# Kernel tuning notes

Hardware: AMD Instinct MI355X
Metric: run time of the kernel (lower is better)

Reference implementation:

```python
import jax, jax.numpy as jnp
import numpy as np

SR = 44100.0
MIN_GAIN, MAX_GAIN = -48.0, 12.0
MIN_EQ, MAX_EQ = -15.0, 15.0
MIN_CTS, MAX_CTS = -20.0, 10.0
# Freeverb (JUCE Reverb, as used by pedalboard.Reverb) tunings @ 44.1 kHz
COMB_T = [1116, 1188, 1277, 1356, 1422, 1491, 1557, 1617]
AP_T = [556, 441, 341, 225]
COMB_OFF = [0]
for _L in COMB_T:
    COMB_OFF.append(COMB_OFF[-1] + _L)
AP_OFF = [0]
for _L in AP_T:
    AP_OFF.append(AP_OFF[-1] + _L)


def restore(x, lo, hi):
    # inverse of normalize-to-(0,1)
    return x * (hi - lo) + lo


def first_order(fc, kind):
    # bilinear-transform 1st-order HP/LP (pedalboard High/LowpassFilter are 1st order)
    K = jnp.tan(np.pi * fc / SR)
    a1 = (K - 1.0) / (K + 1.0)
    z = jnp.zeros_like(fc)
    if kind == "hp":
        b0 = 1.0 / (1.0 + K)
        b = jnp.stack([b0, -b0, z], -1)
    else:
        b0 = K / (1.0 + K)
        b = jnp.stack([b0, b0, z], -1)
    a = jnp.stack([jnp.ones_like(fc), a1, z], -1)
    return b, a


def shelf(fc, gain_db, high):
    # RBJ cookbook shelf, Q = 1/sqrt(2)
    A = 10.0 ** (gain_db / 40.0)
    w = 2.0 * np.pi * fc / SR
    cw = jnp.cos(w)
    alpha = jnp.sin(w) * (np.sqrt(2.0) / 2.0)
    sq = 2.0 * jnp.sqrt(A) * alpha
    s = 1.0 if high else -1.0
    b0 = A * ((A + 1.0) + s * (A - 1.0) * cw + sq)
    b1 = -2.0 * s * A * ((A - 1.0) + s * (A + 1.0) * cw)
    b2 = A * ((A + 1.0) + s * (A - 1.0) * cw - sq)
    a0 = (A + 1.0) - s * (A - 1.0) * cw + sq
    a1 = 2.0 * s * ((A - 1.0) - s * (A + 1.0) * cw)
    a2 = (A + 1.0) - s * (A - 1.0) * cw - sq
    return jnp.stack([b0, b1, b2], -1), jnp.stack([a0, a1, a2], -1)


def peak(fc, gain_db, q):
    # RBJ cookbook peaking EQ
    A = 10.0 ** (gain_db / 40.0)
    w = 2.0 * np.pi * fc / SR
    cw = jnp.cos(w)
    alpha = jnp.sin(w) / (2.0 * q)
    b = jnp.stack([1.0 + alpha * A, -2.0 * cw, 1.0 - alpha * A], -1)
    a = jnp.stack([1.0 + alpha / A, -2.0 * cw, 1.0 - alpha / A], -1)
    return b, a


def cascade_biquads(x, B, A):
    # x: [N, T]; B, A: [N, 6, 3]. DF2T cascade of 6 sections via one scan.
    B = B / A[..., :1]
    A = A / A[..., :1]
    n_sec = B.shape[1]

    def step(z, xt):  # z: [N, 6, 2], xt: [N]
        s = xt
        zn = []
        for k in range(n_sec):
            y = B[:, k, 0] * s + z[:, k, 0]
            z1 = B[:, k, 1] * s - A[:, k, 1] * y + z[:, k, 1]
            z2 = B[:, k, 2] * s - A[:, k, 2] * y
            zn.append(jnp.stack([z1, z2], -1))
            s = y
        return jnp.stack(zn, 1), s

    z0 = jnp.zeros((x.shape[0], n_sec, 2), x.dtype)
    _, y = jax.lax.scan(step, z0, x.T)
    return y.T


def compressor(x, thr_db, ratio, att_ms, rel_ms):
    # feed-forward compressor, dB-domain gain computer + one-pole attack/release
    a_att = jnp.exp(-1.0 / (att_ms * 1e-3 * SR))  # [N]
    a_rel = jnp.exp(-1.0 / (rel_ms * 1e-3 * SR))
    lvl = 20.0 * jnp.log10(jnp.abs(x) + 1e-6)  # [N, T]
    tgt = jnp.minimum(0.0, (thr_db[:, None] - lvl) * (1.0 - 1.0 / ratio[:, None]))

    def step(g, t):  # g, t: [N] gain reduction in dB (<= 0)
        coef = jnp.where(t < g, a_att, a_rel)
        g = coef * g + (1.0 - coef) * t
        return g, g

    _, g = jax.lax.scan(step, jnp.zeros(x.shape[0], x.dtype), tgt.T)
    return x * 10.0 ** (g.T / 20.0)


def freeverb(x, room, damp01, wet, dry, width):
    # JUCE/Freeverb mono: 8 parallel damped combs -> 4 series allpasses
    fb = room * 0.28 + 0.7
    damp = damp01 * 0.4
    wet1 = 3.0 * wet * 0.5 * (1.0 + width)
    dryg = 2.0 * dry
    N = x.shape[0]
    CL, AL = COMB_OFF[-1], AP_OFF[-1]

    def step(carry, xt):
        cb, ab, st, t = carry
        inp = xt * 0.015
        acc = jnp.zeros_like(xt)
        st_new = []
        for k in range(8):
            idx = COMB_OFF[k] + t % COMB_T[k]
            out = cb[:, idx]
            s = out * (1.0 - damp) + st[:, k] * damp
            cb = cb.at[:, idx].set(inp + s * fb)
            st_new.append(s)
            acc = acc + out
        for k in range(4):
            idx = AP_OFF[k] + t % AP_T[k]
            buf = ab[:, idx]
            ab = ab.at[:, idx].set(acc + buf * 0.5)
            acc = buf - acc
        y = acc * wet1 + xt * dryg
        return (cb, ab, jnp.stack(st_new, 1), t + 1), y

    carry0 = (jnp.zeros((N, CL), x.dtype), jnp.zeros((N, AL), x.dtype),
              jnp.zeros((N, 8), x.dtype), jnp.int32(0))
    _, y = jax.lax.scan(step, carry0, x.T)
    return y.T


def _forward(x, p):
    bs, nt, T = x.shape
    N = bs * nt
    xf = x.reshape(N, T)
    pf = p.reshape(N, 24)

    gain_in = restore(pf[:, 0], MIN_GAIN, MAX_GAIN)
    xf = xf * (10.0 ** (gain_in / 20.0))[:, None]

    hp_fc = restore(pf[:, 1], 0.0, 350.0)
    lp_fc = restore(pf[:, 2], 3000.0, 22000.0)
    hs_fc = restore(pf[:, 3], 1500.0, 16000.0)
    hs_g = restore(pf[:, 4], MIN_EQ, MAX_EQ)
    ls_fc = restore(pf[:, 5], 30.0, 450.0)
    ls_g = restore(pf[:, 6], MIN_EQ, MAX_EQ)
    mh_fc = restore(pf[:, 7], 600.0, 7000.0)
    mh_g = restore(pf[:, 8], MIN_EQ, MAX_EQ)
    mh_q = restore(pf[:, 9], 0.5, 3.0)
    ml_fc = restore(pf[:, 10], 200.0, 2500.0)
    ml_g = restore(pf[:, 11], MIN_EQ, MAX_EQ)
    ml_q = restore(pf[:, 12], 0.5, 3.0)
    c_thr = restore(pf[:, 13], MIN_CTS, MAX_CTS)
    c_rat = restore(pf[:, 14], 1.0, 20.0)
    c_att = restore(pf[:, 15], 1.0, 30.0)
    c_rel = restore(pf[:, 16], 100.0, 4000.0)

    coefs = [first_order(hp_fc, "hp"), first_order(lp_fc, "lp"),
             shelf(hs_fc, hs_g, True), shelf(ls_fc, ls_g, False),
             peak(mh_fc, mh_g, mh_q), peak(ml_fc, ml_g, ml_q)]
    B = jnp.stack([c[0] for c in coefs], 1)  # [N, 6, 3]
    A = jnp.stack([c[1] for c in coefs], 1)
    xf = cascade_biquads(xf, B, A)
    xf = compressor(xf, c_thr, c_rat, c_att, c_rel)
    xf = freeverb(xf, pf[:, 17], pf[:, 18], pf[:, 19], pf[:, 20], pf[:, 21])

    gain_out = restore(pf[:, 22], MIN_GAIN, MAX_GAIN)
    xf = xf * (10.0 ** (gain_out / 20.0))[:, None]

    pan = restore(pf[:, 23], 0.3, 0.7)
    theta = pan * (np.pi / 2.0)
    pang = jnp.stack([jnp.cos(theta), jnp.sin(theta)], -1).reshape(bs, nt, 2)
    y = jnp.einsum("bnt,bnc->bct", xf.reshape(bs, nt, T), pang)

    p_out = jnp.stack([gain_in, hp_fc, lp_fc, hs_fc, hs_g, ls_fc, ls_g,
                       mh_fc, mh_g, mh_q, ml_fc, ml_g, ml_q,
                       c_thr, c_rat, c_att, c_rel,
                       pf[:, 17], pf[:, 18], pf[:, 19], pf[:, 20], pf[:, 21],
                       gain_out, pan], -1).reshape(bs, nt, 24)
    return y, p_out


_forward_jit = jax.jit(_forward)


def setup_inputs() -> dict:
    key = jax.random.key(0)
    k1, k2 = jax.random.split(key)
    x = 0.1 * jax.random.normal(k1, (4, 8, 65536), dtype=jnp.float32)
    p = jax.random.uniform(k2, (4, 8, 24), dtype=jnp.float32)
    return {"x": x, "p": p}


def reference(x, p):
    return _forward_jit(x, p)
```

## Files before the change

kernel.cpp:

```cpp
#include <hip/hip_runtime.h>
#include <math.h>

#define T 65536
#define NCH 32
#define LCHUNK 512
#define CCHUNK 128
#define SB 256
#define NBLK 256
#define VH 8

#define OFS_A  0
#define OFS_B1 2097152
#define OFS_I  4194304
#define OFS_P  7340032
#define OFS_M  7342080
#define OFS_V  7346688
#define OFS_Z  7395840


__device__ void norm_store(double b0,double b1,double b2,double a0,double a1,double a2,
                           double* B, double* A1, double* A2, int k){
  B[k*3+0]=b0/a0; B[k*3+1]=b1/a0; B[k*3+2]=b2/a0; A1[k]=a1/a0; A2[k]=a2/a0;
}

__device__ void shelf_coefs(double fc, double g, double s, double* B, double* A1, double* A2, int k){
  double A  = pow(10.0, g/40.0);
  double w  = 2.0*3.14159265358979323846*fc/44100.0;
  double cw = cos(w);
  double al = sin(w)*0.70710678118654752;
  double sq = 2.0*sqrt(A)*al;
  double b0 = A*((A+1.0) + s*(A-1.0)*cw + sq);
  double b1 = -2.0*s*A*((A-1.0) + s*(A+1.0)*cw);
  double b2 = A*((A+1.0) + s*(A-1.0)*cw - sq);
  double a0 = (A+1.0) - s*(A-1.0)*cw + sq;
  double a1 = 2.0*s*((A-1.0) - s*(A+1.0)*cw);
  double a2 = (A+1.0) - s*(A-1.0)*cw - sq;
  norm_store(b0,b1,b2,a0,a1,a2,B,A1,A2,k);
}

__device__ void peak_coefs(double fc, double g, double q, double* B, double* A1, double* A2, int k){
  double A  = pow(10.0, g/40.0);
  double w  = 2.0*3.14159265358979323846*fc/44100.0;
  double cw = cos(w);
  double al = sin(w)/(2.0*q);
  norm_store(1.0+al*A, -2.0*cw, 1.0-al*A, 1.0+al/A, -2.0*cw, 1.0-al/A, B,A1,A2,k);
}

__global__ void k_params(const float* __restrict__ p, float* __restrict__ ws, float* __restrict__ pout){
  int ch = threadIdx.x;
  if (ch >= NCH) return;
  const float* pf = p + ch*24;
  float f[24];
  #pragma unroll
  for (int j=0;j<24;j++) f[j]=pf[j];

  double gain_in = (double)f[0]*60.0 - 48.0;
  double hp_fc  = (double)f[1]*350.0;
  double lp_fc  = (double)f[2]*19000.0 + 3000.0;
  double hs_fc  = (double)f[3]*14500.0 + 1500.0;
  double hs_g   = (double)f[4]*30.0 - 15.0;
  double ls_fc  = (double)f[5]*420.0 + 30.0;
  double ls_g   = (double)f[6]*30.0 - 15.0;
  double mh_fc  = (double)f[7]*6400.0 + 600.0;
  double mh_g   = (double)f[8]*30.0 - 15.0;
  double mh_q   = (double)f[9]*2.5 + 0.5;
  double ml_fc  = (double)f[10]*2300.0 + 200.0;
  double ml_g   = (double)f[11]*30.0 - 15.0;
  double ml_q   = (double)f[12]*2.5 + 0.5;
  double c_thr  = (double)f[13]*30.0 - 20.0;
  double c_rat  = (double)f[14]*19.0 + 1.0;
  double c_att  = (double)f[15]*29.0 + 1.0;
  double c_rel  = (double)f[16]*3900.0 + 100.0;
  double gain_out=(double)f[22]*60.0 - 48.0;
  double pan    = (double)f[23]*0.4 + 0.3;

  double B[18], A1[6], A2[6];
  { double K = tan(3.14159265358979323846*hp_fc/44100.0);
    double a1=(K-1.0)/(K+1.0), b0=1.0/(1.0+K);
    B[0]=b0; B[1]=-b0; B[2]=0.0; A1[0]=a1; A2[0]=0.0; }
  { double K = tan(3.14159265358979323846*lp_fc/44100.0);
    double a1=(K-1.0)/(K+1.0), b0=K/(1.0+K);
    B[3]=b0; B[4]=b0; B[5]=0.0; A1[1]=a1; A2[1]=0.0; }
  shelf_coefs(hs_fc, hs_g,  1.0, B, A1, A2, 2);
  shelf_coefs(ls_fc, ls_g, -1.0, B, A1, A2, 3);
  peak_coefs (mh_fc, mh_g, mh_q, B, A1, A2, 4);
  peak_coefs (ml_fc, ml_g, ml_q, B, A1, A2, 5);

  double gin = pow(10.0, gain_in/20.0);
  B[0]*=gin; B[1]*=gin; B[2]*=gin;

  float* Pc = ws + OFS_P + ch*64;
  #pragma unroll
  for (int k=0;k<6;k++){
    Pc[k]    = (float)B[k*3+0];
    Pc[6+k]  = (float)B[k*3+1];
    Pc[12+k] = (float)B[k*3+2];
    Pc[18+k] = (float)A1[k];
    Pc[24+k] = (float)A2[k];
  }
  Pc[30] = (float)c_thr;
  Pc[31] = (float)(1.0 - 1.0/c_rat);
  Pc[32] = (float)exp(-1.0/(c_att*0.001*44100.0));
  Pc[33] = (float)exp(-1.0/(c_rel*0.001*44100.0));
  double fb   = (double)f[17]*0.28 + 0.7;
  double damp = (double)f[18]*0.4;
  double wet1 = 3.0*(double)f[19]*0.5*(1.0+(double)f[21]);
  double dryg = 2.0*(double)f[20];
  double gout = pow(10.0, gain_out/20.0);
  Pc[34] = (float)fb;
  Pc[35] = (float)damp;
  Pc[36] = (float)(wet1*gout);
  Pc[37] = (float)(dryg*gout/0.015);
  Pc[38] = (float)cos(pan*1.57079632679489662);
  Pc[39] = (float)sin(pan*1.57079632679489662);

  float* po = pout + ch*24;
  po[0]=(float)gain_in; po[1]=(float)hp_fc; po[2]=(float)lp_fc; po[3]=(float)hs_fc;
  po[4]=(float)hs_g; po[5]=(float)ls_fc; po[6]=(float)ls_g; po[7]=(float)mh_fc;
  po[8]=(float)mh_g; po[9]=(float)mh_q; po[10]=(float)ml_fc; po[11]=(float)ml_g;
  po[12]=(float)ml_q; po[13]=(float)c_thr; po[14]=(float)c_rat; po[15]=(float)c_att;
  po[16]=(float)c_rel; po[17]=f[17]; po[18]=f[18]; po[19]=f[19]; po[20]=f[20];
  po[21]=f[21]; po[22]=(float)gain_out; po[23]=(float)pan;
}


__device__ __forceinline__ float bq_step(const float* b0, const float* b1, const float* b2,
                                         const float* a1, const float* a2,
                                         float* z1, float* z2, float s){
  #pragma unroll
  for (int k=0;k<6;k++){
    float y = fmaf(b0[k], s, z1[k]);
    z1[k] = fmaf(b1[k], s, fmaf(-a1[k], y, z2[k]));
    z2[k] = fmaf(b2[k], s, -a2[k]*y);
    s = y;
  }
  return s;
}

__device__ __forceinline__ void load_coefs(const float* Pc, float* b0, float* b1, float* b2,
                                           float* a1, float* a2){
  #pragma unroll
  for (int k=0;k<6;k++){
    b0[k]=Pc[k]; b1[k]=Pc[6+k]; b2[k]=Pc[12+k]; a1[k]=Pc[18+k]; a2[k]=Pc[24+k];
  }
}

__global__ void k_chunk1(const float* __restrict__ x, float* __restrict__ ws){
  int tg = blockIdx.x*64 + threadIdx.x;
  int ch = tg / 140, sub = tg % 140;
  if (ch >= NCH) return;
  const float* Pc = ws + OFS_P + ch*64;
  float b0[6],b1[6],b2[6],a1[6],a2[6];
  load_coefs(Pc,b0,b1,b2,a1,a2);
  float z1[6]={0,0,0,0,0,0}, z2[6]={0,0,0,0,0,0};

  if (sub < CCHUNK){
    const float4* xp = (const float4*)(x + ch*T + sub*LCHUNK);
    for (int j=0;j<LCHUNK/4;j++){
      float4 v = xp[j];
      bq_step(b0,b1,b2,a1,a2,z1,z2,v.x);
      bq_step(b0,b1,b2,a1,a2,z1,z2,v.y);
      bq_step(b0,b1,b2,a1,a2,z1,z2,v.z);
      bq_step(b0,b1,b2,a1,a2,z1,z2,v.w);
    }
    float* vo = ws + OFS_V + (ch*CCHUNK + sub)*12;
    #pragma unroll
    for (int k=0;k<6;k++){ vo[2*k]=z1[k]; vo[2*k+1]=z2[k]; }
  } else {
    int j = sub - CCHUNK;
    if ((j & 1)==0) z1[j>>1]=1.0f; else z2[j>>1]=1.0f;
    for (int t=0;t<LCHUNK;t++) bq_step(b0,b1,b2,a1,a2,z1,z2,0.0f);
    float* mo = ws + OFS_M + ch*144 + j*12;
    #pragma unroll
    for (int k=0;k<6;k++){ mo[2*k]=z1[k]; mo[2*k+1]=z2[k]; }
  }
}

__global__ void k_chunk2(float* __restrict__ ws){
  int ch = threadIdx.x;
  if (ch >= NCH) return;
  const float* M = ws + OFS_M + ch*144;
  const float* V = ws + OFS_V + ch*CCHUNK*12;
  float*       Z = ws + OFS_Z + ch*CCHUNK*12;
  float z[12];
  #pragma unroll
  for (int i=0;i<12;i++) z[i]=0.0f;
  for (int c=0;c<CCHUNK;c++){
    #pragma unroll
    for (int i=0;i<12;i++) Z[c*12+i]=z[i];
    float zn[12];
    #pragma unroll
    for (int i=0;i<12;i++) zn[i]=V[c*12+i];
    #pragma unroll
    for (int j=0;j<12;j++){
      float zj = z[j];
      #pragma unroll
      for (int i=0;i<12;i++) zn[i] = fmaf(M[j*12+i], zj, zn[i]);
    }
    #pragma unroll
    for (int i=0;i<12;i++) z[i]=zn[i];
  }
}

__global__ void k_chunk3(const float* __restrict__ x, float* __restrict__ ws){
  int tg = blockIdx.x*64 + threadIdx.x;
  int ch = tg >> 7, c = tg & (CCHUNK-1);
  const float* Pc = ws + OFS_P + ch*64;
  float b0[6],b1[6],b2[6],a1[6],a2[6];
  load_coefs(Pc,b0,b1,b2,a1,a2);
  float thr = Pc[30], rt = Pc[31];
  float aA = Pc[32], aR = Pc[33];
  float kA = 1.0f - aA, kR = 1.0f - aR;
  const float* Zi = ws + OFS_Z + (ch*CCHUNK + c)*12;
  float z1[6], z2[6];
  #pragma unroll
  for (int k=0;k<6;k++){ z1[k]=Zi[2*k]; z2[k]=Zi[2*k+1]; }
  const float4* xp = (const float4*)(x + ch*T + c*LCHUNK);
  float4* Ao  = (float4*)(ws + OFS_A  + (size_t)ch*T + c*LCHUNK);
  float4* B1o = (float4*)(ws + OFS_B1 + (size_t)ch*T + c*LCHUNK);
  float*  Ig  = ws + OFS_I + (size_t)ch*98304;

  for (int gg=0; gg<64; gg++){
    float4 v0 = xp[2*gg], v1 = xp[2*gg+1];
    float ya[8], Tv[8];
    ya[0]=bq_step(b0,b1,b2,a1,a2,z1,z2,v0.x);
    ya[1]=bq_step(b0,b1,b2,a1,a2,z1,z2,v0.y);
    ya[2]=bq_step(b0,b1,b2,a1,a2,z1,z2,v0.z);
    ya[3]=bq_step(b0,b1,b2,a1,a2,z1,z2,v0.w);
    ya[4]=bq_step(b0,b1,b2,a1,a2,z1,z2,v1.x);
    ya[5]=bq_step(b0,b1,b2,a1,a2,z1,z2,v1.y);
    ya[6]=bq_step(b0,b1,b2,a1,a2,z1,z2,v1.z);
    ya[7]=bq_step(b0,b1,b2,a1,a2,z1,z2,v1.w);
    #pragma unroll
    for (int s=0;s<8;s++)
      Tv[s] = fminf(0.0f, (thr - 6.0205999132796239f*log2f(fabsf(ya[s])+1e-6f))*rt);
    Ao[2*gg]   = make_float4(ya[0],ya[1],ya[2],ya[3]);
    Ao[2*gg+1] = make_float4(ya[4],ya[5],ya[6],ya[7]);
    B1o[2*gg]   = make_float4(Tv[0],Tv[1],Tv[2],Tv[3]);
    B1o[2*gg+1] = make_float4(Tv[4],Tv[5],Tv[6],Tv[7]);
    float bb[9];
    bb[0] = kR*Tv[0]; bb[1] = kA*Tv[0];
    #pragma unroll
    for (int s=1;s<8;s++){
      float bA = kA*Tv[s], bR = kR*Tv[s];
      bb[s+1] = fmaf(aA, bb[s], bA);
      #pragma unroll
      for (int j=7;j>=1;j--){
        if (j<=s) bb[j] = fminf(fmaf(aA, bb[j-1], bA), fmaf(aR, bb[j], bR));
      }
      bb[0] = fmaf(aR, bb[0], bR);
    }
    int G = c*64 + gg;
    float* ig = Ig + (G>>5)*384 + (G&31)*12;
    *(float4*)(ig)   = make_float4(bb[0],bb[1],bb[2],bb[3]);
    *(float4*)(ig+4) = make_float4(bb[4],bb[5],bb[6],bb[7]);
    *(float4*)(ig+8) = make_float4(bb[8],0.0f,0.0f,0.0f);
  }
}


__global__ __launch_bounds__(320) void k_verb(float* __restrict__ ws){
  const int LC[8] = {1116,1188,1277,1356,1422,1491,1557,1617};
  const int COFF[8] = {0,1116,2304,3581,4937,6359,7850,9407};
  const int LA[4] = {556,441,341,225};
  const int AOFF[4] = {0,556,997,1338};
  int ch = blockIdx.x, tid = threadIdx.x;
  __shared__ float cb[11024];
  __shared__ float ab[1563];
  __shared__ float cH[8][264];
  __shared__ float xts[256];
  __shared__ float B1st[2][256];
  __shared__ float IldS[384];
  __shared__ float gB[2][32];
  __shared__ float xfer[32];
  const float* Pc = ws + OFS_P + ch*64;
  float fb = Pc[34], damp = Pc[35], wet1 = Pc[36], dryk = Pc[37];
  float aA = Pc[32], aR = Pc[33];
  float kA = 1.0f - aA, kR = 1.0f - aR;
  float omd = 1.0f - damp;
  float* Aio = ws + OFS_A + (size_t)ch*T;
  const float* B1c = ws + OFS_B1 + (size_t)ch*T;
  const float* IG  = ws + OFS_I + (size_t)ch*98304;
  for (int i=tid;i<11024;i+=320) cb[i]=0.0f;
  for (int i=tid;i<1563;i+=320)  ab[i]=0.0f;
  for (int i=tid;i<8*264;i+=320) ((float*)cH)[i]=0.0f;
  bool scanw = (tid >= 256);
  int sl = tid - 256;
  float w[VH];
  { float pw = 1.0f;
    #pragma unroll
    for (int d=0;d<VH;d++){ w[d]=pw; pw*=damp; } }
  float sj[9];
  { float pA = 1.0f;
    #pragma unroll
    for (int j=0;j<9;j++){ sj[j]=pA; pA*=aA; }
    float pR = 1.0f;
    #pragma unroll
    for (int j=8;j>=0;j--){ sj[j]*=pR; pR*=aR; } }
  int cbb[8] = {0,0,0,0,0,0,0,0};
  int abb[4] = {0,0,0,0};
  float gcarry = 0.0f;
  float4 iR0, iR1, bR;
  float xv = 0.0f;

  if (scanw){
    const float4* isrc = (const float4*)(IG);
    float4* idst = (float4*)IldS;
    idst[sl] = isrc[sl];
    if (sl < 32) idst[64+sl] = isrc[64+sl];
    iR0 = isrc[96+sl];
    if (sl < 32) iR1 = isrc[96+64+sl];
    const float4* bsrc = (const float4*)(B1c);
    ((float4*)B1st[0])[sl] = bsrc[sl];
    ((float4*)B1st[1])[sl] = bsrc[64+sl];
  }
  if (tid < 256) xv = Aio[tid];
  __syncthreads();
  if (tid == 256){
    float g = 0.0f;
    for (int m=0;m<32;m++){
      gB[0][m] = g;
      const float* Ip = &IldS[m*12];
      float f0=fmaf(sj[0],g,Ip[0]), f1=fmaf(sj[1],g,Ip[1]), f2=fmaf(sj[2],g,Ip[2]);
      float f3=fmaf(sj[3],g,Ip[3]), f4=fmaf(sj[4],g,Ip[4]), f5=fmaf(sj[5],g,Ip[5]);
      float f6=fmaf(sj[6],g,Ip[6]), f7=fmaf(sj[7],g,Ip[7]), f8=fmaf(sj[8],g,Ip[8]);
      g = fminf(fminf(fminf(f0,f1),fminf(f2,f3)),
                fminf(fminf(f4,f5),fminf(fminf(f6,f7),f8)));
    }
    gcarry = g;
  }
  __syncthreads();

  for (int i=0;i<NBLK;i++){
    int t0 = i<<8;
    int p = i & 1;
    float xt = 0.0f, acc = 0.0f, a = 0.0f;
    if (tid < 256){
      int m = tid>>3, r = tid&7;
      float g = gB[p][m];
      const float* Bl = B1st[p] + (m<<3);
      float4 q0 = *(const float4*)(Bl);
      float4 q1 = *(const float4*)(Bl+4);
      float tv[8] = {q0.x,q0.y,q0.z,q0.w,q1.x,q1.y,q1.z,q1.w};
      #pragma unroll
      for (int s=0;s<8;s++){
        if (s<=r){
          float tt = tv[s];
          g = fminf(fmaf(aA,g,kA*tt), fmaf(aR,g,kR*tt));
        }
      }
      xt = xv * exp2f(g*0.16609640474436813f) * 0.015f;
      xts[tid] = xt;
      #pragma unroll
      for (int k=0;k<8;k++){
        int idx = cbb[k]+tid; if (idx>=LC[k]) idx-=LC[k];
        float o = cb[COFF[k]+idx];
        cH[k][VH+tid] = omd*o;
        acc += o;
      }
    } else if (i+1 < NBLK){
      float4* idst = (float4*)IldS;
      idst[sl] = iR0;
      if (sl < 32) idst[64+sl] = iR1;
      if (i >= 1) ((float4*)B1st[(i+1)&1])[sl] = bR;
    }
    __syncthreads();
    if (tid < 256){
      if (i+1 < NBLK) xv = Aio[t0+256+tid];
      #pragma unroll
      for (int k=0;k<8;k++){
        float s = 0.0f;
        #pragma unroll
        for (int d=0;d<VH;d++) s = fmaf(w[d], cH[k][VH+tid-d], s);
        int idx = cbb[k]+tid; if (idx>=LC[k]) idx-=LC[k];
        cb[COFF[k]+idx] = fmaf(fb, s, xt);
      }
      a = acc;
      #pragma unroll
      for (int j=0;j<3;j++){
        int idx = abb[j]+tid; if (idx>=LA[j]) idx-=LA[j];
        float bv = ab[AOFF[j]+idx];
        ab[AOFF[j]+idx] = fmaf(0.5f, bv, a);
        a = bv - a;
      }
      if (tid >= 225) xfer[tid-225] = a;
    } else {
      if (i+2 < NBLK){
        const float4* isrc = (const float4*)(IG + (size_t)(i+2)*384);
        iR0 = isrc[sl];
        if (sl < 32) iR1 = isrc[64+sl];
        const float4* bsrc = (const float4*)(B1c + (size_t)(i+2)*SB);
        bR = bsrc[sl];
      }
      if (tid == 256 && i+1 < NBLK){
        int q = (i+1)&1;
        float g = gcarry;
        #pragma unroll 4
        for (int m=0;m<32;m++){
          gB[q][m] = g;
          const float* Ip = &IldS[m*12];
          float f0=fmaf(sj[0],g,Ip[0]), f1=fmaf(sj[1],g,Ip[1]), f2=fmaf(sj[2],g,Ip[2]);
          float f3=fmaf(sj[3],g,Ip[3]), f4=fmaf(sj[4],g,Ip[4]), f5=fmaf(sj[5],g,Ip[5]);
          float f6=fmaf(sj[6],g,Ip[6]), f7=fmaf(sj[7],g,Ip[7]), f8=fmaf(sj[8],g,Ip[8]);
          g = fminf(fminf(fminf(f0,f1),fminf(f2,f3)),
                    fminf(fminf(f4,f5),fminf(fminf(f6,f7),f8)));
        }
        gcarry = g;
      }
    }
    __syncthreads();
    if (tid < 225){
      int idx = abb[3]+tid; if (idx>=225) idx-=225;
      float bv = ab[AOFF[3]+idx];
      float b  = fmaf(0.5f, bv, a);
      float y  = bv - a;
      Aio[t0+tid] = fmaf(y, wet1, xts[tid]*dryk);
      if (tid < 31){
        float a2 = xfer[tid];
        float y2 = b - a2;
        ab[AOFF[3]+idx] = fmaf(0.5f, b, a2);
        Aio[t0+225+tid] = fmaf(y2, wet1, xts[225+tid]*dryk);
      } else {
        ab[AOFF[3]+idx] = b;
      }
    } else if (tid >= 232 && tid < 288){
      int q = tid-232; int k = q/7, d = q%7;
      cH[k][1+d] = cH[k][257+d];
    }
    #pragma unroll
    for (int k=0;k<8;k++){ cbb[k]+=SB; if (cbb[k]>=LC[k]) cbb[k]-=LC[k]; }
    #pragma unroll
    for (int j=0;j<4;j++){
      abb[j]+=SB;
      if (abb[j]>=LA[j]) abb[j]-=LA[j];
      if (abb[j]>=LA[j]) abb[j]-=LA[j];
    }
    __syncthreads();
  }
}


__global__ void k_mix(const float* __restrict__ ws, float* __restrict__ out){
  int id = blockIdx.x*256 + threadIdx.x;
  int t = id & (T-1), b = id >> 16;
  const float* Av = ws + OFS_A + (size_t)b*8*T + t;
  const float* P = ws + OFS_P;
  float s0=0.0f, s1=0.0f;
  #pragma unroll
  for (int n=0;n<8;n++){
    float v = Av[(size_t)n*T];
    int ch = b*8+n;
    s0 = fmaf(v, P[ch*64+38], s0);
    s1 = fmaf(v, P[ch*64+39], s1);
  }
  out[b*2*T + t]     = s0;
  out[b*2*T + T + t] = s1;
}

extern "C" void kernel_launch(void* const* d_in, const int* in_sizes, int n_in,
                              void* d_out, int out_size, void* d_ws, size_t ws_size,
                              hipStream_t stream) {
  const float* x = (const float*)d_in[0];
  const float* p = (const float*)d_in[1];
  float* out = (float*)d_out;
  float* ws  = (float*)d_ws;

  k_params<<<1, 64, 0, stream>>>(p, ws, out + 4*2*T);
  k_chunk1<<<70, 64, 0, stream>>>(x, ws);
  k_chunk2<<<1, 64, 0, stream>>>(ws);
  k_chunk3<<<64, 64, 0, stream>>>(x, ws);
  k_verb  <<<NCH, 320, 0, stream>>>(ws);
  k_mix   <<<(4*T)/256, 256, 0, stream>>>(ws, out);
}
```

Before: 962.5 us.

## Restructure reverb block loop to two barriers with padded comb buffers and split scan

Result: slower. 1.087 ms (+13.0%).

```diff
diff --git a/kernel.cpp b/kernel.cpp
--- a/kernel.cpp
+++ b/kernel.cpp
@@ -145,7 +145,7 @@
   }
 }
 
-__global__ void k_chunk1(const float* __restrict__ x, float* __restrict__ ws){
+__global__ __launch_bounds__(64,1) void k_chunk1(const float* __restrict__ x, float* __restrict__ ws){
   int tg = blockIdx.x*64 + threadIdx.x;
   int ch = tg / 140, sub = tg % 140;
   if (ch >= NCH) return;
@@ -176,33 +176,42 @@
   }
 }
 
-__global__ void k_chunk2(float* __restrict__ ws){
+__global__ __launch_bounds__(64,1) void k_chunk2(float* __restrict__ ws){
   int ch = threadIdx.x;
   if (ch >= NCH) return;
   const float* M = ws + OFS_M + ch*144;
   const float* V = ws + OFS_V + ch*CCHUNK*12;
   float*       Z = ws + OFS_Z + ch*CCHUNK*12;
-  float z[12];
+  float Mr[144];
+  #pragma unroll
+  for (int i=0;i<144;i++) Mr[i]=M[i];
+  float z[12], vbuf[12];
   #pragma unroll
   for (int i=0;i<12;i++) z[i]=0.0f;
+  #pragma unroll
+  for (int i=0;i<12;i++) vbuf[i]=V[i];
   for (int c=0;c<CCHUNK;c++){
     #pragma unroll
     for (int i=0;i<12;i++) Z[c*12+i]=z[i];
     float zn[12];
     #pragma unroll
-    for (int i=0;i<12;i++) zn[i]=V[c*12+i];
+    for (int i=0;i<12;i++) zn[i]=vbuf[i];
+    if (c+1<CCHUNK){
+      #pragma unroll
+      for (int i=0;i<12;i++) vbuf[i]=V[(c+1)*12+i];
+    }
     #pragma unroll
     for (int j=0;j<12;j++){
       float zj = z[j];
       #pragma unroll
-      for (int i=0;i<12;i++) zn[i] = fmaf(M[j*12+i], zj, zn[i]);
+      for (int i=0;i<12;i++) zn[i] = fmaf(Mr[j*12+i], zj, zn[i]);
     }
     #pragma unroll
     for (int i=0;i<12;i++) z[i]=zn[i];
   }
 }
 
-__global__ void k_chunk3(const float* __restrict__ x, float* __restrict__ ws){
+__global__ __launch_bounds__(64,1) void k_chunk3(const float* __restrict__ x, float* __restrict__ ws){
   int tg = blockIdx.x*64 + threadIdx.x;
   int ch = tg >> 7, c = tg & (CCHUNK-1);
   const float* Pc = ws + OFS_P + ch*64;
@@ -259,20 +268,33 @@
 }
 
 
+__device__ __forceinline__ float scan_run(const float* I, const float* sj, float g,
+                                          float* grow, int m0, int m1){
+  #pragma unroll 4
+  for (int m=m0;m<m1;m++){
+    grow[m]=g;
+    const float* Ip=&I[m*12];
+    float f0=fmaf(sj[0],g,Ip[0]), f1=fmaf(sj[1],g,Ip[1]), f2=fmaf(sj[2],g,Ip[2]);
+    float f3=fmaf(sj[3],g,Ip[3]), f4=fmaf(sj[4],g,Ip[4]), f5=fmaf(sj[5],g,Ip[5]);
+    float f6=fmaf(sj[6],g,Ip[6]), f7=fmaf(sj[7],g,Ip[7]), f8=fmaf(sj[8],g,Ip[8]);
+    g = fminf(fminf(fminf(f0,f1),fminf(f2,f3)),
+              fminf(fminf(f4,f5),fminf(fminf(f6,f7),f8)));
+  }
+  return g;
+}
+
 __global__ __launch_bounds__(320) void k_verb(float* __restrict__ ws){
   const int LC[8] = {1116,1188,1277,1356,1422,1491,1557,1617};
-  const int COFF[8] = {0,1116,2304,3581,4937,6359,7850,9407};
+  const int CPF[8] = {0,1124,2320,3605,4969,6399,7898,9463};
   const int LA[4] = {556,441,341,225};
   const int AOFF[4] = {0,556,997,1338};
   int ch = blockIdx.x, tid = threadIdx.x;
-  __shared__ float cb[11024];
+  __shared__ float cb[11088];
   __shared__ float ab[1563];
-  __shared__ float cH[8][264];
-  __shared__ float xts[256];
+  __shared__ float haloS[2][8][8];
   __shared__ float B1st[2][256];
   __shared__ float IldS[384];
-  __shared__ float gB[2][32];
-  __shared__ float xfer[32];
+  __shared__ float gB[3][32];
   const float* Pc = ws + OFS_P + ch*64;
   float fb = Pc[34], damp = Pc[35], wet1 = Pc[36], dryk = Pc[37];
   float aA = Pc[32], aR = Pc[33];
@@ -281,13 +303,13 @@
   float* Aio = ws + OFS_A + (size_t)ch*T;
   const float* B1c = ws + OFS_B1 + (size_t)ch*T;
   const float* IG  = ws + OFS_I + (size_t)ch*98304;
-  for (int i=tid;i<11024;i+=320) cb[i]=0.0f;
+  for (int i=tid;i<11088;i+=320) cb[i]=0.0f;
   for (int i=tid;i<1563;i+=320)  ab[i]=0.0f;
-  for (int i=tid;i<8*264;i+=320) ((float*)cH)[i]=0.0f;
+  if (tid < 128) ((float*)haloS)[tid]=0.0f;
   bool scanw = (tid >= 256);
   int sl = tid - 256;
   float w[VH];
-  { float pw = 1.0f;
+  { float pw = omd;
     #pragma unroll
     for (int d=0;d<VH;d++){ w[d]=pw; pw*=damp; } }
   float sj[9];
@@ -301,43 +323,47 @@
   int abb[4] = {0,0,0,0};
   float gcarry = 0.0f;
   float4 iR0, iR1, bR;
-  float xv = 0.0f;
+  float xv = 0.0f, xvn = 0.0f;
+  float aH = 0.0f, xtH = 0.0f; int idxH = 0;
 
   if (scanw){
     const float4* isrc = (const float4*)(IG);
     float4* idst = (float4*)IldS;
     idst[sl] = isrc[sl];
     if (sl < 32) idst[64+sl] = isrc[64+sl];
-    iR0 = isrc[96+sl];
-    if (sl < 32) iR1 = isrc[96+64+sl];
     const float4* bsrc = (const float4*)(B1c);
     ((float4*)B1st[0])[sl] = bsrc[sl];
     ((float4*)B1st[1])[sl] = bsrc[64+sl];
-  }
-  if (tid < 256) xv = Aio[tid];
+    if (sl == 0) gcarry = scan_run(IldS, sj, 0.0f, gB[0], 0, 32);
+    idst[sl] = isrc[96+sl];
+    if (sl < 32) idst[64+sl] = isrc[96+64+sl];
+    if (sl == 0) gcarry = scan_run(IldS, sj, gcarry, gB[1], 0, 32);
+    iR0 = isrc[192+sl];
+    if (sl < 32) iR1 = isrc[192+64+sl];
+    bR = ((const float4*)(B1c + 2*SB))[sl];
+  } else {
+    xv = Aio[tid];
+  }
   __syncthreads();
-  if (tid == 256){
-    float g = 0.0f;
-    for (int m=0;m<32;m++){
-      gB[0][m] = g;
-      const float* Ip = &IldS[m*12];
-      float f0=fmaf(sj[0],g,Ip[0]), f1=fmaf(sj[1],g,Ip[1]), f2=fmaf(sj[2],g,Ip[2]);
-      float f3=fmaf(sj[3],g,Ip[3]), f4=fmaf(sj[4],g,Ip[4]), f5=fmaf(sj[5],g,Ip[5]);
-      float f6=fmaf(sj[6],g,Ip[6]), f7=fmaf(sj[7],g,Ip[7]), f8=fmaf(sj[8],g,Ip[8]);
-      g = fminf(fminf(fminf(f0,f1),fminf(f2,f3)),
-                fminf(fminf(f4,f5),fminf(fminf(f6,f7),f8)));
-    }
-    gcarry = g;
-  }
-  __syncthreads();
-
+
+  int pr = 0, pw2 = 2;
   for (int i=0;i<NBLK;i++){
     int t0 = i<<8;
     int p = i & 1;
-    float xt = 0.0f, acc = 0.0f, a = 0.0f;
+    float acc = 0.0f, xt = 0.0f, a = 0.0f, outv = 0.0f, nb4v = 0.0f;
+    float wv[8]; int qk[8];
+    float nb1=0.f, nb2=0.f, nb3=0.f, bv4=0.f;
+    int idx1=0, idx2=0, idx3=0, idx4=0;
     if (tid < 256){
+      if (i > 0 && tid >= 225){
+        float bv = ab[AOFF[3]+idxH];
+        float y  = bv - aH;
+        ab[AOFF[3]+idxH] = fmaf(0.5f, bv, aH);
+        Aio[t0-256+tid] = fmaf(y, wet1, xtH*dryk);
+      }
+      if (i+1 < NBLK) xvn = Aio[t0+256+tid];
       int m = tid>>3, r = tid&7;
-      float g = gB[p][m];
+      float g = gB[pr][m];
       const float* Bl = B1st[p] + (m<<3);
       float4 q0 = *(const float4*)(Bl);
       float4 q1 = *(const float4*)(Bl+4);
@@ -350,82 +376,86 @@
         }
       }
       xt = xv * exp2f(g*0.16609640474436813f) * 0.015f;
-      xts[tid] = xt;
       #pragma unroll
       for (int k=0;k<8;k++){
-        int idx = cbb[k]+tid; if (idx>=LC[k]) idx-=LC[k];
-        float o = cb[COFF[k]+idx];
-        cH[k][VH+tid] = omd*o;
+        int slot = cbb[k]+tid; if (slot>=LC[k]) slot-=LC[k];
+        int q = CPF[k] + 8 + slot;
+        qk[k] = q;
+        const float* bp = &cb[q-7];
+        float f0=bp[0],f1=bp[1],f2=bp[2],f3=bp[3],f4=bp[4],f5=bp[5],f6=bp[6],f7=bp[7];
+        if (tid < 7){
+          f0 = haloS[p][k][tid];
+          if (tid<6) f1 = haloS[p][k][tid+1];
+          if (tid<5) f2 = haloS[p][k][tid+2];
+          if (tid<4) f3 = haloS[p][k][tid+3];
+          if (tid<3) f4 = haloS[p][k][tid+4];
+          if (tid<2) f5 = haloS[p][k][tid+5];
+          if (tid<1) f6 = haloS[p][k][tid+6];
+        }
+        float o = f7;
         acc += o;
-      }
-    } else if (i+1 < NBLK){
-      float4* idst = (float4*)IldS;
-      idst[sl] = iR0;
-      if (sl < 32) idst[64+sl] = iR1;
-      if (i >= 1) ((float4*)B1st[(i+1)&1])[sl] = bR;
+        float s = (fmaf(w[0],f7,w[1]*f6) + fmaf(w[2],f5,w[3]*f4))
+                + (fmaf(w[4],f3,w[5]*f2) + fmaf(w[6],f1,w[7]*f0));
+        wv[k] = fmaf(fb, s, xt);
+        if (tid >= 249) haloS[p^1][k][tid-249] = o;
+      }
+      idx1 = abb[0]+tid; if (idx1>=LA[0]) idx1-=LA[0];
+      idx2 = abb[1]+tid; if (idx2>=LA[1]) idx2-=LA[1];
+      idx3 = abb[2]+tid; if (idx3>=LA[2]) idx3-=LA[2];
+      idx4 = abb[3]+tid; if (idx4>=225) idx4-=225; if (idx4>=225) idx4-=225;
+      float bv1 = ab[AOFF[0]+idx1];
+      float bv2 = ab[AOFF[1]+idx2];
+      float bv3 = ab[AOFF[2]+idx3];
+      if (tid < 194) bv4 = ab[AOFF[3]+idx4];
+      a = acc;
+      nb1 = fmaf(0.5f, bv1, a); a = bv1 - a;
+      nb2 = fmaf(0.5f, bv2, a); a = bv2 - a;
+      nb3 = fmaf(0.5f, bv3, a); a = bv3 - a;
+      if (tid < 194){
+        nb4v = fmaf(0.5f, bv4, a);
+        float y = bv4 - a;
+        outv = fmaf(y, wet1, xt*dryk);
+      }
+    } else {
+      if (i+2 < NBLK){
+        float4* idst = (float4*)IldS;
+        idst[sl] = iR0;
+        if (sl < 32) idst[64+sl] = iR1;
+      }
+      if (i >= 1 && i+1 < NBLK) ((float4*)B1st[(i+1)&1])[sl] = bR;
+      if (tid == 256 && i+2 < NBLK) gcarry = scan_run(IldS, sj, gcarry, gB[pw2], 0, 16);
     }
     __syncthreads();
     if (tid < 256){
-      if (i+1 < NBLK) xv = Aio[t0+256+tid];
       #pragma unroll
       for (int k=0;k<8;k++){
-        float s = 0.0f;
-        #pragma unroll
-        for (int d=0;d<VH;d++) s = fmaf(w[d], cH[k][VH+tid-d], s);
-        int idx = cbb[k]+tid; if (idx>=LC[k]) idx-=LC[k];
-        cb[COFF[k]+idx] = fmaf(fb, s, xt);
-      }
-      a = acc;
-      #pragma unroll
-      for (int j=0;j<3;j++){
-        int idx = abb[j]+tid; if (idx>=LA[j]) idx-=LA[j];
-        float bv = ab[AOFF[j]+idx];
-        ab[AOFF[j]+idx] = fmaf(0.5f, bv, a);
-        a = bv - a;
-      }
-      if (tid >= 225) xfer[tid-225] = a;
+        cb[qk[k]] = wv[k];
+        int slot = qk[k] - CPF[k] - 8;
+        if (slot >= LC[k]-7) cb[qk[k]-LC[k]] = wv[k];
+      }
+      ab[AOFF[0]+idx1] = nb1;
+      ab[AOFF[1]+idx2] = nb2;
+      ab[AOFF[2]+idx3] = nb3;
+      if (tid < 194){
+        ab[AOFF[3]+idx4] = nb4v;
+        Aio[t0+tid] = outv;
+      } else if (tid < 225){
+        float bv = ab[AOFF[3]+idx4];
+        float y  = bv - a;
+        ab[AOFF[3]+idx4] = fmaf(0.5f, bv, a);
+        Aio[t0+tid] = fmaf(y, wet1, xt*dryk);
+      } else {
+        aH = a; idxH = idx4; xtH = xt;
+      }
+      xv = xvn;
     } else {
-      if (i+2 < NBLK){
-        const float4* isrc = (const float4*)(IG + (size_t)(i+2)*384);
+      if (i+3 < NBLK){
+        const float4* isrc = (const float4*)(IG + (size_t)(i+3)*384);
         iR0 = isrc[sl];
         if (sl < 32) iR1 = isrc[64+sl];
-        const float4* bsrc = (const float4*)(B1c + (size_t)(i+2)*SB);
-        bR = bsrc[sl];
-      }
-      if (tid == 256 && i+1 < NBLK){
-        int q = (i+1)&1;
-        float g = gcarry;
-        #pragma unroll 4
-        for (int m=0;m<32;m++){
-          gB[q][m] = g;
-          const float* Ip = &IldS[m*12];
-          float f0=fmaf(sj[0],g,Ip[0]), f1=fmaf(sj[1],g,Ip[1]), f2=fmaf(sj[2],g,Ip[2]);
-          float f3=fmaf(sj[3],g,Ip[3]), f4=fmaf(sj[4],g,Ip[4]), f5=fmaf(sj[5],g,Ip[5]);
-          float f6=fmaf(sj[6],g,Ip[6]), f7=fmaf(sj[7],g,Ip[7]), f8=fmaf(sj[8],g,Ip[8]);
-          g = fminf(fminf(fminf(f0,f1),fminf(f2,f3)),
-                    fminf(fminf(f4,f5),fminf(fminf(f6,f7),f8)));
-        }
-        gcarry = g;
-      }
-    }
-    __syncthreads();
-    if (tid < 225){
-      int idx = abb[3]+tid; if (idx>=225) idx-=225;
-      float bv = ab[AOFF[3]+idx];
-      float b  = fmaf(0.5f, bv, a);
-      float y  = bv - a;
-      Aio[t0+tid] = fmaf(y, wet1, xts[tid]*dryk);
-      if (tid < 31){
-        float a2 = xfer[tid];
-        float y2 = b - a2;
-        ab[AOFF[3]+idx] = fmaf(0.5f, b, a2);
-        Aio[t0+225+tid] = fmaf(y2, wet1, xts[225+tid]*dryk);
-      } else {
-        ab[AOFF[3]+idx] = b;
-      }
-    } else if (tid >= 232 && tid < 288){
-      int q = tid-232; int k = q/7, d = q%7;
-      cH[k][1+d] = cH[k][257+d];
+      }
+      if (i+2 < NBLK) bR = ((const float4*)(B1c + (size_t)(i+2)*SB))[sl];
+      if (tid == 256 && i+2 < NBLK) gcarry = scan_run(IldS, sj, gcarry, gB[pw2], 16, 32);
     }
     #pragma unroll
     for (int k=0;k<8;k++){ cbb[k]+=SB; if (cbb[k]>=LC[k]) cbb[k]-=LC[k]; }
@@ -435,7 +465,14 @@
       if (abb[j]>=LA[j]) abb[j]-=LA[j];
       if (abb[j]>=LA[j]) abb[j]-=LA[j];
     }
+    pr++; if (pr==3) pr=0;
+    pw2++; if (pw2==3) pw2=0;
     __syncthreads();
+  }
+  if (tid >= 225 && tid < 256){
+    float bv = ab[AOFF[3]+idxH];
+    float y  = bv - aH;
+    Aio[((NBLK-1)<<8)+tid] = fmaf(y, wet1, xtH*dryk);
   }
 }
 
```

## Pack two reverb channels per block and cache transition matrix in registers

Applied to the files above, without the earlier changes.

New measurement: 1.317 ms. 36.8% more time.

```diff
diff --git a/kernel.cpp b/kernel.cpp
--- a/kernel.cpp
+++ b/kernel.cpp
@@ -145,7 +145,7 @@
   }
 }
 
-__global__ void k_chunk1(const float* __restrict__ x, float* __restrict__ ws){
+__global__ __launch_bounds__(64,1) void k_chunk1(const float* __restrict__ x, float* __restrict__ ws){
   int tg = blockIdx.x*64 + threadIdx.x;
   int ch = tg / 140, sub = tg % 140;
   if (ch >= NCH) return;
@@ -176,33 +176,42 @@
   }
 }
 
-__global__ void k_chunk2(float* __restrict__ ws){
+__global__ __launch_bounds__(64,1) void k_chunk2(float* __restrict__ ws){
   int ch = threadIdx.x;
   if (ch >= NCH) return;
   const float* M = ws + OFS_M + ch*144;
   const float* V = ws + OFS_V + ch*CCHUNK*12;
   float*       Z = ws + OFS_Z + ch*CCHUNK*12;
-  float z[12];
+  float Mr[144];
+  #pragma unroll
+  for (int i=0;i<144;i++) Mr[i]=M[i];
+  float z[12], vbuf[12];
   #pragma unroll
   for (int i=0;i<12;i++) z[i]=0.0f;
+  #pragma unroll
+  for (int i=0;i<12;i++) vbuf[i]=V[i];
   for (int c=0;c<CCHUNK;c++){
     #pragma unroll
     for (int i=0;i<12;i++) Z[c*12+i]=z[i];
     float zn[12];
     #pragma unroll
-    for (int i=0;i<12;i++) zn[i]=V[c*12+i];
+    for (int i=0;i<12;i++) zn[i]=vbuf[i];
+    if (c+1<CCHUNK){
+      #pragma unroll
+      for (int i=0;i<12;i++) vbuf[i]=V[(c+1)*12+i];
+    }
     #pragma unroll
     for (int j=0;j<12;j++){
       float zj = z[j];
       #pragma unroll
-      for (int i=0;i<12;i++) zn[i] = fmaf(M[j*12+i], zj, zn[i]);
+      for (int i=0;i<12;i++) zn[i] = fmaf(Mr[j*12+i], zj, zn[i]);
     }
     #pragma unroll
     for (int i=0;i<12;i++) z[i]=zn[i];
   }
 }
 
-__global__ void k_chunk3(const float* __restrict__ x, float* __restrict__ ws){
+__global__ __launch_bounds__(64,1) void k_chunk3(const float* __restrict__ x, float* __restrict__ ws){
   int tg = blockIdx.x*64 + threadIdx.x;
   int ch = tg >> 7, c = tg & (CCHUNK-1);
   const float* Pc = ws + OFS_P + ch*64;
@@ -259,20 +268,27 @@
 }
 
 
-__global__ __launch_bounds__(320) void k_verb(float* __restrict__ ws){
+#define CSTRIDE 15948
+
+__global__ __launch_bounds__(640) void k_verb(float* __restrict__ ws){
   const int LC[8] = {1116,1188,1277,1356,1422,1491,1557,1617};
   const int COFF[8] = {0,1116,2304,3581,4937,6359,7850,9407};
   const int LA[4] = {556,441,341,225};
   const int AOFF[4] = {0,556,997,1338};
-  int ch = blockIdx.x, tid = threadIdx.x;
-  __shared__ float cb[11024];
-  __shared__ float ab[1563];
-  __shared__ float cH[8][264];
-  __shared__ float xts[256];
-  __shared__ float B1st[2][256];
-  __shared__ float IldS[384];
-  __shared__ float gB[2][32];
-  __shared__ float xfer[32];
+  extern __shared__ float smem[];
+  int tid = threadIdx.x;
+  int half = tid / 320;
+  int ltid = tid - half*320;
+  int ch = blockIdx.x*2 + half;
+  float* S    = smem + half*CSTRIDE;
+  float* IldS = S;
+  float* B1stA= S + 384;
+  float* cb   = S + 896;
+  float* ab   = S + 11920;
+  float* cHf  = S + 13483;
+  float* xts  = S + 15595;
+  float* gBf  = S + 15851;
+  float* xfer = S + 15915;
   const float* Pc = ws + OFS_P + ch*64;
   float fb = Pc[34], damp = Pc[35], wet1 = Pc[36], dryk = Pc[37];
   float aA = Pc[32], aR = Pc[33];
@@ -281,11 +297,11 @@
   float* Aio = ws + OFS_A + (size_t)ch*T;
   const float* B1c = ws + OFS_B1 + (size_t)ch*T;
   const float* IG  = ws + OFS_I + (size_t)ch*98304;
-  for (int i=tid;i<11024;i+=320) cb[i]=0.0f;
-  for (int i=tid;i<1563;i+=320)  ab[i]=0.0f;
-  for (int i=tid;i<8*264;i+=320) ((float*)cH)[i]=0.0f;
-  bool scanw = (tid >= 256);
-  int sl = tid - 256;
+  for (int i=ltid;i<11024;i+=320) cb[i]=0.0f;
+  for (int i=ltid;i<1563;i+=320)  ab[i]=0.0f;
+  for (int i=ltid;i<8*264;i+=320) cHf[i]=0.0f;
+  bool scanw = (ltid >= 256);
+  int sl = ltid - 256;
   float w[VH];
   { float pw = 1.0f;
     #pragma unroll
@@ -311,15 +327,15 @@
     iR0 = isrc[96+sl];
     if (sl < 32) iR1 = isrc[96+64+sl];
     const float4* bsrc = (const float4*)(B1c);
-    ((float4*)B1st[0])[sl] = bsrc[sl];
-    ((float4*)B1st[1])[sl] = bsrc[64+sl];
-  }
-  if (tid < 256) xv = Aio[tid];
+    ((float4*)B1stA)[sl] = bsrc[sl];
+    ((float4*)(B1stA+256))[sl] = bsrc[64+sl];
+  }
+  if (ltid < 256) xv = Aio[ltid];
   __syncthreads();
-  if (tid == 256){
+  if (ltid == 256){
     float g = 0.0f;
     for (int m=0;m<32;m++){
-      gB[0][m] = g;
+      gBf[m] = g;
       const float* Ip = &IldS[m*12];
       float f0=fmaf(sj[0],g,Ip[0]), f1=fmaf(sj[1],g,Ip[1]), f2=fmaf(sj[2],g,Ip[2]);
       float f3=fmaf(sj[3],g,Ip[3]), f4=fmaf(sj[4],g,Ip[4]), f5=fmaf(sj[5],g,Ip[5]);
@@ -335,10 +351,10 @@
     int t0 = i<<8;
     int p = i & 1;
     float xt = 0.0f, acc = 0.0f, a = 0.0f;
-    if (tid < 256){
-      int m = tid>>3, r = tid&7;
-      float g = gB[p][m];
-      const float* Bl = B1st[p] + (m<<3);
+    if (ltid < 256){
+      int m = ltid>>3, r = ltid&7;
+      float g = gBf[p*32+m];
+      const float* Bl = B1stA + p*256 + (m<<3);
       float4 q0 = *(const float4*)(Bl);
       float4 q1 = *(const float4*)(Bl+4);
       float tv[8] = {q0.x,q0.y,q0.z,q0.w,q1.x,q1.y,q1.z,q1.w};
@@ -350,40 +366,40 @@
         }
       }
       xt = xv * exp2f(g*0.16609640474436813f) * 0.015f;
-      xts[tid] = xt;
+      xts[ltid] = xt;
       #pragma unroll
       for (int k=0;k<8;k++){
-        int idx = cbb[k]+tid; if (idx>=LC[k]) idx-=LC[k];
+        int idx = cbb[k]+ltid; if (idx>=LC[k]) idx-=LC[k];
         float o = cb[COFF[k]+idx];
-        cH[k][VH+tid] = omd*o;
+        cHf[k*264+VH+ltid] = omd*o;
         acc += o;
       }
     } else if (i+1 < NBLK){
       float4* idst = (float4*)IldS;
       idst[sl] = iR0;
       if (sl < 32) idst[64+sl] = iR1;
-      if (i >= 1) ((float4*)B1st[(i+1)&1])[sl] = bR;
+      if (i >= 1) ((float4*)(B1stA+((i+1)&1)*256))[sl] = bR;
     }
     __syncthreads();
-    if (tid < 256){
-      if (i+1 < NBLK) xv = Aio[t0+256+tid];
+    if (ltid < 256){
+      if (i+1 < NBLK) xv = Aio[t0+256+ltid];
       #pragma unroll
       for (int k=0;k<8;k++){
         float s = 0.0f;
         #pragma unroll
-        for (int d=0;d<VH;d++) s = fmaf(w[d], cH[k][VH+tid-d], s);
-        int idx = cbb[k]+tid; if (idx>=LC[k]) idx-=LC[k];
+        for (int d=0;d<VH;d++) s = fmaf(w[d], cHf[k*264+VH+ltid-d], s);
+        int idx = cbb[k]+ltid; if (idx>=LC[k]) idx-=LC[k];
         cb[COFF[k]+idx] = fmaf(fb, s, xt);
       }
       a = acc;
       #pragma unroll
       for (int j=0;j<3;j++){
-        int idx = abb[j]+tid; if (idx>=LA[j]) idx-=LA[j];
+        int idx = abb[j]+ltid; if (idx>=LA[j]) idx-=LA[j];
         float bv = ab[AOFF[j]+idx];
         ab[AOFF[j]+idx] = fmaf(0.5f, bv, a);
         a = bv - a;
       }
-      if (tid >= 225) xfer[tid-225] = a;
+      if (ltid >= 225) xfer[ltid-225] = a;
     } else {
       if (i+2 < NBLK){
         const float4* isrc = (const float4*)(IG + (size_t)(i+2)*384);
@@ -392,12 +408,12 @@
         const float4* bsrc = (const float4*)(B1c + (size_t)(i+2)*SB);
         bR = bsrc[sl];
       }
-      if (tid == 256 && i+1 < NBLK){
+      if (ltid == 256 && i+1 < NBLK){
         int q = (i+1)&1;
         float g = gcarry;
         #pragma unroll 4
         for (int m=0;m<32;m++){
-          gB[q][m] = g;
+          gBf[q*32+m] = g;
           const float* Ip = &IldS[m*12];
           float f0=fmaf(sj[0],g,Ip[0]), f1=fmaf(sj[1],g,Ip[1]), f2=fmaf(sj[2],g,Ip[2]);
           float f3=fmaf(sj[3],g,Ip[3]), f4=fmaf(sj[4],g,Ip[4]), f5=fmaf(sj[5],g,Ip[5]);
@@ -409,23 +425,23 @@
       }
     }
     __syncthreads();
-    if (tid < 225){
-      int idx = abb[3]+tid; if (idx>=225) idx-=225;
+    if (ltid < 225){
+      int idx = abb[3]+ltid; if (idx>=225) idx-=225;
       float bv = ab[AOFF[3]+idx];
       float b  = fmaf(0.5f, bv, a);
       float y  = bv - a;
-      Aio[t0+tid] = fmaf(y, wet1, xts[tid]*dryk);
-      if (tid < 31){
-        float a2 = xfer[tid];
+      Aio[t0+ltid] = fmaf(y, wet1, xts[ltid]*dryk);
+      if (ltid < 31){
+        float a2 = xfer[ltid];
         float y2 = b - a2;
         ab[AOFF[3]+idx] = fmaf(0.5f, b, a2);
-        Aio[t0+225+tid] = fmaf(y2, wet1, xts[225+tid]*dryk);
+        Aio[t0+225+ltid] = fmaf(y2, wet1, xts[225+ltid]*dryk);
       } else {
         ab[AOFF[3]+idx] = b;
       }
-    } else if (tid >= 232 && tid < 288){
-      int q = tid-232; int k = q/7, d = q%7;
-      cH[k][1+d] = cH[k][257+d];
+    } else if (ltid >= 232 && ltid < 288){
+      int q = ltid-232; int k = q/7, d = q%7;
+      cHf[k*264+1+d] = cHf[k*264+257+d];
     }
     #pragma unroll
     for (int k=0;k<8;k++){ cbb[k]+=SB; if (cbb[k]>=LC[k]) cbb[k]-=LC[k]; }
@@ -465,10 +481,13 @@
   float* out = (float*)d_out;
   float* ws  = (float*)d_ws;
 
+  (void)hipFuncSetAttribute((const void*)k_verb,
+                            hipFuncAttributeMaxDynamicSharedMemorySize, 131072);
+
   k_params<<<1, 64, 0, stream>>>(p, ws, out + 4*2*T);
   k_chunk1<<<70, 64, 0, stream>>>(x, ws);
   k_chunk2<<<1, 64, 0, stream>>>(ws);
   k_chunk3<<<64, 64, 0, stream>>>(x, ws);
-  k_verb  <<<NCH, 320, 0, stream>>>(ws);
+  k_verb  <<<NCH/2, 640, 2*CSTRIDE*4, stream>>>(ws);
   k_mix   <<<(4*T)/256, 256, 0, stream>>>(ws, out);
 }
```

## Split reverb comb filters across extra warps and cache chunk matrix in registers

Applied to the files above, without the earlier changes.

New measurement: 1.030 ms. 1.07x slower.

```diff
diff --git a/kernel.cpp b/kernel.cpp
--- a/kernel.cpp
+++ b/kernel.cpp
@@ -145,7 +145,7 @@
   }
 }
 
-__global__ void k_chunk1(const float* __restrict__ x, float* __restrict__ ws){
+__global__ __launch_bounds__(64,1) void k_chunk1(const float* __restrict__ x, float* __restrict__ ws){
   int tg = blockIdx.x*64 + threadIdx.x;
   int ch = tg / 140, sub = tg % 140;
   if (ch >= NCH) return;
@@ -176,33 +176,42 @@
   }
 }
 
-__global__ void k_chunk2(float* __restrict__ ws){
+__global__ __launch_bounds__(64,1) void k_chunk2(float* __restrict__ ws){
   int ch = threadIdx.x;
   if (ch >= NCH) return;
   const float* M = ws + OFS_M + ch*144;
   const float* V = ws + OFS_V + ch*CCHUNK*12;
   float*       Z = ws + OFS_Z + ch*CCHUNK*12;
-  float z[12];
+  float Mr[144];
+  #pragma unroll
+  for (int i=0;i<144;i++) Mr[i]=M[i];
+  float z[12], vbuf[12];
   #pragma unroll
   for (int i=0;i<12;i++) z[i]=0.0f;
+  #pragma unroll
+  for (int i=0;i<12;i++) vbuf[i]=V[i];
   for (int c=0;c<CCHUNK;c++){
     #pragma unroll
     for (int i=0;i<12;i++) Z[c*12+i]=z[i];
     float zn[12];
     #pragma unroll
-    for (int i=0;i<12;i++) zn[i]=V[c*12+i];
+    for (int i=0;i<12;i++) zn[i]=vbuf[i];
+    if (c+1<CCHUNK){
+      #pragma unroll
+      for (int i=0;i<12;i++) vbuf[i]=V[(c+1)*12+i];
+    }
     #pragma unroll
     for (int j=0;j<12;j++){
       float zj = z[j];
       #pragma unroll
-      for (int i=0;i<12;i++) zn[i] = fmaf(M[j*12+i], zj, zn[i]);
+      for (int i=0;i<12;i++) zn[i] = fmaf(Mr[j*12+i], zj, zn[i]);
     }
     #pragma unroll
     for (int i=0;i<12;i++) z[i]=zn[i];
   }
 }
 
-__global__ void k_chunk3(const float* __restrict__ x, float* __restrict__ ws){
+__global__ __launch_bounds__(64,1) void k_chunk3(const float* __restrict__ x, float* __restrict__ ws){
   int tg = blockIdx.x*64 + threadIdx.x;
   int ch = tg >> 7, c = tg & (CCHUNK-1);
   const float* Pc = ws + OFS_P + ch*64;
@@ -259,7 +268,7 @@
 }
 
 
-__global__ __launch_bounds__(320) void k_verb(float* __restrict__ ws){
+__global__ __launch_bounds__(576) void k_verb(float* __restrict__ ws){
   const int LC[8] = {1116,1188,1277,1356,1422,1491,1557,1617};
   const int COFF[8] = {0,1116,2304,3581,4937,6359,7850,9407};
   const int LA[4] = {556,441,341,225};
@@ -269,6 +278,7 @@
   __shared__ float ab[1563];
   __shared__ float cH[8][264];
   __shared__ float xts[256];
+  __shared__ float accH[256];
   __shared__ float B1st[2][256];
   __shared__ float IldS[384];
   __shared__ float gB[2][32];
@@ -281,11 +291,14 @@
   float* Aio = ws + OFS_A + (size_t)ch*T;
   const float* B1c = ws + OFS_B1 + (size_t)ch*T;
   const float* IG  = ws + OFS_I + (size_t)ch*98304;
-  for (int i=tid;i<11024;i+=320) cb[i]=0.0f;
-  for (int i=tid;i<1563;i+=320)  ab[i]=0.0f;
-  for (int i=tid;i<8*264;i+=320) ((float*)cH)[i]=0.0f;
-  bool scanw = (tid >= 256);
-  int sl = tid - 256;
+  for (int i=tid;i<11024;i+=576) cb[i]=0.0f;
+  for (int i=tid;i<1563;i+=576)  ab[i]=0.0f;
+  for (int i=tid;i<8*264;i+=576) ((float*)cH)[i]=0.0f;
+  bool loww  = (tid < 256);
+  bool highw = (tid >= 256 && tid < 512);
+  bool scanw = (tid >= 512);
+  int hs = tid - 256;
+  int sl = tid - 512;
   float w[VH];
   { float pw = 1.0f;
     #pragma unroll
@@ -314,9 +327,9 @@
     ((float4*)B1st[0])[sl] = bsrc[sl];
     ((float4*)B1st[1])[sl] = bsrc[64+sl];
   }
-  if (tid < 256) xv = Aio[tid];
+  if (loww) xv = Aio[tid];
   __syncthreads();
-  if (tid == 256){
+  if (tid == 512){
     float g = 0.0f;
     for (int m=0;m<32;m++){
       gB[0][m] = g;
@@ -335,7 +348,7 @@
     int t0 = i<<8;
     int p = i & 1;
     float xt = 0.0f, acc = 0.0f, a = 0.0f;
-    if (tid < 256){
+    if (loww){
       int m = tid>>3, r = tid&7;
       float g = gB[p][m];
       const float* Bl = B1st[p] + (m<<3);
@@ -352,12 +365,22 @@
       xt = xv * exp2f(g*0.16609640474436813f) * 0.015f;
       xts[tid] = xt;
       #pragma unroll
-      for (int k=0;k<8;k++){
+      for (int k=0;k<4;k++){
         int idx = cbb[k]+tid; if (idx>=LC[k]) idx-=LC[k];
         float o = cb[COFF[k]+idx];
         cH[k][VH+tid] = omd*o;
         acc += o;
       }
+    } else if (highw){
+      float acc4 = 0.0f;
+      #pragma unroll
+      for (int k=4;k<8;k++){
+        int idx = cbb[k]+hs; if (idx>=LC[k]) idx-=LC[k];
+        float o = cb[COFF[k]+idx];
+        cH[k][VH+hs] = omd*o;
+        acc4 += o;
+      }
+      accH[hs] = acc4;
     } else if (i+1 < NBLK){
       float4* idst = (float4*)IldS;
       idst[sl] = iR0;
@@ -365,17 +388,17 @@
       if (i >= 1) ((float4*)B1st[(i+1)&1])[sl] = bR;
     }
     __syncthreads();
-    if (tid < 256){
+    if (loww){
       if (i+1 < NBLK) xv = Aio[t0+256+tid];
       #pragma unroll
-      for (int k=0;k<8;k++){
+      for (int k=0;k<4;k++){
         float s = 0.0f;
         #pragma unroll
         for (int d=0;d<VH;d++) s = fmaf(w[d], cH[k][VH+tid-d], s);
         int idx = cbb[k]+tid; if (idx>=LC[k]) idx-=LC[k];
         cb[COFF[k]+idx] = fmaf(fb, s, xt);
       }
-      a = acc;
+      a = acc + accH[tid];
       #pragma unroll
       for (int j=0;j<3;j++){
         int idx = abb[j]+tid; if (idx>=LA[j]) idx-=LA[j];
@@ -384,6 +407,16 @@
         a = bv - a;
       }
       if (tid >= 225) xfer[tid-225] = a;
+    } else if (highw){
+      float xth = xts[hs];
+      #pragma unroll
+      for (int k=4;k<8;k++){
+        float s = 0.0f;
+        #pragma unroll
+        for (int d=0;d<VH;d++) s = fmaf(w[d], cH[k][VH+hs-d], s);
+        int idx = cbb[k]+hs; if (idx>=LC[k]) idx-=LC[k];
+        cb[COFF[k]+idx] = fmaf(fb, s, xth);
+      }
     } else {
       if (i+2 < NBLK){
         const float4* isrc = (const float4*)(IG + (size_t)(i+2)*384);
@@ -392,7 +425,7 @@
         const float4* bsrc = (const float4*)(B1c + (size_t)(i+2)*SB);
         bR = bsrc[sl];
       }
-      if (tid == 256 && i+1 < NBLK){
+      if (tid == 512 && i+1 < NBLK){
         int q = (i+1)&1;
         float g = gcarry;
         #pragma unroll 4
@@ -469,6 +502,6 @@
   k_chunk1<<<70, 64, 0, stream>>>(x, ws);
   k_chunk2<<<1, 64, 0, stream>>>(ws);
   k_chunk3<<<64, 64, 0, stream>>>(x, ws);
-  k_verb  <<<NCH, 320, 0, stream>>>(ws);
+  k_verb  <<<NCH, 576, 0, stream>>>(ws);
   k_mix   <<<(4*T)/256, 256, 0, stream>>>(ws, out);
 }
```
